# Kernel optimization log

Measured on AMD Instinct MI355X. Metric: run time of the kernel, lower is better.

The kernel has to match this reference:

```python
import jax, jax.numpy as jnp
import numpy as np

N_STATE = 256   # complex state size n (real state is 2n)
N_IN = 128
BATCH = 16
T_STEPS = 2048
H_STEP = 0.01
EPS = 1e-3
LAM_RE_MIN, LAM_RE_MAX, MAX_PHASE = -5.0, -0.5, 6.283


def setup_inputs() -> dict:
    rng = np.random.default_rng(0)
    n, nu = N_STATE, N_IN
    # trainable params (as in torch __init__)
    u1 = rng.random(n)
    u2 = rng.random(n) * 2.0 - 1.0
    alpha = np.log(-(u1 * (LAM_RE_MAX - LAM_RE_MIN) + LAM_RE_MIN)).astype(np.float32)
    theta = (MAX_PHASE * u2).astype(np.float32)
    B_re = (rng.standard_normal((n, nu)) / np.sqrt(2.0 * nu)).astype(np.float32)
    B_im = (rng.standard_normal((n, nu)) / np.sqrt(2.0 * nu)).astype(np.float32)
    # fixed basis-change buffers: rho (normalized), T_inv, P = rho @ T_inv, Pinv
    H1 = rng.standard_normal((n, n))
    H2 = rng.standard_normal((n, n))
    rho = np.block([[H1, -H2], [H2, H1]])
    rho = rho / np.linalg.norm(rho)
    I = np.eye(n)
    T_inv = (1.0 / np.sqrt(2.0)) * np.block([[I, I], [-1j * I, 1j * I]])
    P = rho.astype(np.complex128) @ T_inv
    Pinv = np.linalg.inv(P)
    key = jax.random.key(0)
    k1, k2 = jax.random.split(key)
    return {
        "xi_init": jax.random.normal(k1, (BATCH, 1, 2 * n), dtype=jnp.float32),
        "u_log": jax.random.normal(k2, (BATCH, T_STEPS, nu), dtype=jnp.float32),
        "alpha": jnp.asarray(alpha),
        "theta": jnp.asarray(theta),
        "B_re": jnp.asarray(B_re),
        "B_im": jnp.asarray(B_im),
        "P_re": jnp.asarray(P.real, dtype=jnp.float32),
        "P_im": jnp.asarray(P.imag, dtype=jnp.float32),
        "Pinv_re": jnp.asarray(Pinv.real, dtype=jnp.float32),
        "Pinv_im": jnp.asarray(Pinv.imag, dtype=jnp.float32),
        "T": T_STEPS,
    }


def reference(xi_init, u_log, alpha, theta, B_re, B_im, P_re, P_im, Pinv_re, Pinv_im, T):
    n = alpha.shape[0]
    lam = (-jnp.exp(alpha) - EPS) + 1j * theta          # (n,) complex64
    Bc = B_re + 1j * B_im                               # (n, nu)
    P = P_re + 1j * P_im                                # (2n, 2n)
    Pinv = Pinv_re + 1j * Pinv_im                       # (2n, 2n)
    xi0 = xi_init[:, 0, :]                              # (B, 2n) real

    def step(xi, u_t):
        # xi: (B, 2n) real state; u_t: (B, nu)
        x_tilde = xi.astype(jnp.complex64) @ Pinv.T     # (B, 2n) complex
        x_bar = x_tilde[:, :n]                          # (B, n)
        x_bar_dot = lam * x_bar + u_t.astype(jnp.complex64) @ Bc.T
        x_tilde_dot = jnp.concatenate([x_bar_dot, jnp.conj(x_bar_dot)], axis=-1)
        x_dot = (x_tilde_dot @ P.T).real                # (B, 2n)
        xi_new = xi + H_STEP * x_dot
        return xi_new, xi_new

    u_seq = jnp.swapaxes(u_log, 0, 1)                   # (T, B, nu)
    _, xs = jax.lax.scan(step, xi0, u_seq)              # (T, B, 2n)
    # torch _sim logs xi_init, then skips xi after t=0, logs xi after t=1..T-1
    x_log = jnp.concatenate([xi0[None], xs[1:]], axis=0)  # (T, B, 2n)
    return jnp.swapaxes(x_log, 0, 1)                    # (B, T, 2n)
```

## Files before the change

kernel.cpp:

```cpp
#include <hip/hip_runtime.h>
#include <hip/hip_bf16.h>
#include <cstddef>
#include <cstdint>

#define N_ST 256
#define TWO_N 512
#define NU 128
#define BATCH 16
#define TSTEPS 2048
#define MTOT (BATCH * TSTEPS)
#define H_STEP 0.01f
#define EPS_V 0.001f
#define NCHUNK 32
#define CHUNKL 64

typedef __attribute__((ext_vector_type(4))) float f32x4;
typedef __attribute__((ext_vector_type(4))) short s16x4;
typedef __attribute__((ext_vector_type(8))) short s16x8;

#define OFF_FPK    0
#define OFF_ZPK    8388608
#define OFF_UPK    16777216
#define OFF_WT     18874368
#define OFF_WF     19005440
#define OFF_D      19038208
#define OFF_XBAR0  19039232
#define OFF_E      19047424

static __device__ __forceinline__ float bf2f(short s) {
    return __uint_as_float(((unsigned)(unsigned short)s) << 16);
}

__global__ __launch_bounds__(256) void prep_all(
    const float* __restrict__ P_re, const float* __restrict__ P_im,
    const float* __restrict__ B_re, const float* __restrict__ B_im,
    const float* __restrict__ alpha, const float* __restrict__ theta,
    short* __restrict__ Wtpk, short* __restrict__ Wfpk,
    float* __restrict__ dbuf)
{
    int blk = blockIdx.x, tid = threadIdx.x;
    if (blk < 1024) {
        int idx = blk * 256 + tid;
        int j = idx >> 9, c = idx & 511;
        float v;
        if (c < N_ST) v = P_re[j * TWO_N + c] + P_re[j * TWO_N + c + N_ST];
        else          v = P_im[j * TWO_N + c] - P_im[j * TWO_N + c - N_ST];
        __hip_bfloat16 b = __float2bfloat16(v);
        Wtpk[((size_t)(j >> 4) * TWO_N + c) * 16 + (j & 15)] = *(short*)&b;
    } else if (blk < 1280) {
        int idx = (blk - 1024) * 256 + tid;
        int k = idx >> 9, c = idx & 511;
        float v = (c < N_ST) ? B_re[c * NU + k] : B_im[(c - N_ST) * NU + k];
        __hip_bfloat16 b = __float2bfloat16(H_STEP * v);
        Wfpk[((size_t)(c >> 4) * NU + k) * 16 + (c & 15)] = *(short*)&b;
    } else {
        int i = tid;
        float dr = 1.0f + H_STEP * (-expf(alpha[i]) - EPS_V);
        float di = H_STEP * theta[i];
        float pr = 1.0f, pi = 0.0f;
        for (int k = 0; k < CHUNKL; ++k) { float nr = pr * dr - pi * di; pi = pr * di + pi * dr; pr = nr; }
        dbuf[i] = dr; dbuf[N_ST + i] = di; dbuf[2 * N_ST + i] = pr; dbuf[3 * N_ST + i] = pi;
    }
}

__global__ __launch_bounds__(256) void xbar0_kernel(
    const float* __restrict__ Pinv_re, const float* __restrict__ Pinv_im,
    const float* __restrict__ xi0, float* __restrict__ xbar0)
{
    __shared__ float xs[BATCH * TWO_N];
    int tid = threadIdx.x;
#pragma unroll
    for (int q = 0; q < 8; ++q)
        *reinterpret_cast<float4*>(&xs[(q * 256 + tid) * 4]) =
            *reinterpret_cast<const float4*>(&xi0[(q * 256 + tid) * 4]);
    __syncthreads();

    int wv = tid >> 6, l = tid & 63;
    int i = blockIdx.x * 4 + wv;
    float rp[BATCH] = {}, ip[BATCH] = {};
#pragma unroll
    for (int q = 0; q < 8; ++q) {
        int j = q * 64 + l;
        float pr = Pinv_re[(size_t)i * TWO_N + j];
        float pi = Pinv_im[(size_t)i * TWO_N + j];
#pragma unroll
        for (int b = 0; b < BATCH; ++b) {
            float x = xs[b * TWO_N + j];
            rp[b] = fmaf(pr, x, rp[b]);
            ip[b] = fmaf(pi, x, ip[b]);
        }
    }
#pragma unroll
    for (int m = 1; m < 64; m <<= 1) {
#pragma unroll
        for (int b = 0; b < BATCH; ++b) {
            rp[b] += __shfl_xor(rp[b], m, 64);
            ip[b] += __shfl_xor(ip[b], m, 64);
        }
    }
    if (l == 0) {
#pragma unroll
        for (int b = 0; b < BATCH; ++b) {
            xbar0[b * TWO_N + i] = rp[b];
            xbar0[b * TWO_N + N_ST + i] = ip[b];
        }
    }
}

__global__ __launch_bounds__(256) void upack(const float* __restrict__ u, short* __restrict__ upk) {
    __shared__ short st[64 * 132];
    int tid = threadIdx.x, bid = blockIdx.x;
    const float* up = u + (size_t)bid * 8192;
#pragma unroll
    for (int q = 0; q < 8; ++q) {
        int idx = q * 1024 + tid * 4;
        float4 v = *reinterpret_cast<const float4*>(up + idx);
        int m = idx >> 7, k = idx & 127;
        s16x4 pv;
        __hip_bfloat16 b0 = __float2bfloat16(v.x); pv[0] = *(short*)&b0;
        __hip_bfloat16 b1 = __float2bfloat16(v.y); pv[1] = *(short*)&b1;
        __hip_bfloat16 b2 = __float2bfloat16(v.z); pv[2] = *(short*)&b2;
        __hip_bfloat16 b3 = __float2bfloat16(v.w); pv[3] = *(short*)&b3;
        *reinterpret_cast<__shared__ s16x4*>(&st[m * 132 + k]) = pv;
    }
    __syncthreads();
    short* op = upk + (size_t)bid * 8192;
#pragma unroll
    for (int q2 = 0; q2 < 4; ++q2) {
        int o = q2 * 2048 + tid * 8;
        int ml = o & 15, k = (o >> 4) & 127, sl = o >> 11;
        s16x8 w;
#pragma unroll
        for (int r = 0; r < 8; ++r) w[r] = st[(sl * 16 + ml + r) * 132 + k];
        *reinterpret_cast<s16x8*>(op + o) = w;
    }
}

template <int K, bool PACKOUT>
__global__ __launch_bounds__(512, 2) void gemm_mfma(const short* __restrict__ Apk,
                                                    const short* __restrict__ Bpk,
                                                    float* __restrict__ Cf,
                                                    short* __restrict__ Cp,
                                                    const float* __restrict__ xi0) {
    __shared__ __align__(1024) short lds[32768];
    const int tid = threadIdx.x;
    const int wid = tid >> 6, lane = tid & 63;
    const int l = blockIdx.x;
    const int mb = ((l >> 4) << 3) | (l & 7);
    const int nb = (l >> 3) & 1;
    const int m0 = mb * 256, n0 = nb * 256;
    const int wm = wid >> 2, wn = wid & 3;
    f32x4 acc[8][4] = {};
    const size_t slabStride = (size_t)K * 16;
    const unsigned ldsBase = (unsigned)(uintptr_t)(__attribute__((address_space(3))) short*)&lds[0];
    constexpr int NT = K / 32;

#define STAGE(buf, kk)                                                                              \
    do {                                                                                            \
        const short* gA0 = Apk + ((size_t)(m0 >> 4) + wid)     * slabStride + (size_t)(kk) * 16 + lane * 8; \
        const short* gA1 = Apk + ((size_t)(m0 >> 4) + wid + 8) * slabStride + (size_t)(kk) * 16 + lane * 8; \
        const short* gB0 = Bpk + ((size_t)(n0 >> 4) + wid)     * slabStride + (size_t)(kk) * 16 + lane * 8; \
        const short* gB1 = Bpk + ((size_t)(n0 >> 4) + wid + 8) * slabStride + (size_t)(kk) * 16 + lane * 8; \
        __builtin_amdgcn_global_load_lds((const __attribute__((address_space(1))) void*)gA0,        \
            (__attribute__((address_space(3))) void*)&lds[(buf) * 8192 + wid * 512], 16, 0, 0);     \
        __builtin_amdgcn_global_load_lds((const __attribute__((address_space(1))) void*)gA1,        \
            (__attribute__((address_space(3))) void*)&lds[(buf) * 8192 + (wid + 8) * 512], 16, 0, 0); \
        __builtin_amdgcn_global_load_lds((const __attribute__((address_space(1))) void*)gB0,        \
            (__attribute__((address_space(3))) void*)&lds[16384 + (buf) * 8192 + wid * 512], 16, 0, 0); \
        __builtin_amdgcn_global_load_lds((const __attribute__((address_space(1))) void*)gB1,        \
            (__attribute__((address_space(3))) void*)&lds[16384 + (buf) * 8192 + (wid + 8) * 512], 16, 0, 0); \
    } while (0)

    STAGE(0, 0);

#pragma unroll
    for (int t = 0; t < NT; ++t) {
        const int cur = t & 1;
        if (t + 1 < NT) STAGE(cur ^ 1, (t + 1) * 32);

        if (t + 1 < NT) asm volatile("s_waitcnt vmcnt(4)" ::: "memory");
        else            asm volatile("s_waitcnt vmcnt(0)" ::: "memory");
        __builtin_amdgcn_sched_barrier(0);
        __builtin_amdgcn_s_barrier();
        __builtin_amdgcn_sched_barrier(0);

        s16x4 al[8], ah[8], bl[4], bh[4];
        const unsigned aB = ldsBase + (unsigned)cur * 16384u;
        const unsigned bB = ldsBase + 32768u + (unsigned)cur * 16384u;
#pragma unroll
        for (int i = 0; i < 8; ++i) {
            unsigned ad = aB + ((unsigned)(wm * 8 + i) << 10) + ((unsigned)lane << 3);
            asm volatile("ds_read_b64_tr_b16 %0, %1 offset:0"   : "=v"(al[i]) : "v"(ad));
            asm volatile("ds_read_b64_tr_b16 %0, %1 offset:512" : "=v"(ah[i]) : "v"(ad));
        }
#pragma unroll
        for (int j = 0; j < 4; ++j) {
            unsigned bd = bB + ((unsigned)(wn * 4 + j) << 10) + ((unsigned)lane << 3);
            asm volatile("ds_read_b64_tr_b16 %0, %1 offset:0"   : "=v"(bl[j]) : "v"(bd));
            asm volatile("ds_read_b64_tr_b16 %0, %1 offset:512" : "=v"(bh[j]) : "v"(bd));
        }
        asm volatile("s_waitcnt lgkmcnt(0)" ::: "memory");
        __builtin_amdgcn_sched_barrier(0);
        __builtin_amdgcn_s_barrier();
        __builtin_amdgcn_sched_barrier(0);

        __builtin_amdgcn_s_setprio(1);
#pragma unroll
        for (int i = 0; i < 8; ++i) {
            s16x8 av = __builtin_shufflevector(al[i], ah[i], 0, 1, 2, 3, 4, 5, 6, 7);
#pragma unroll
            for (int j = 0; j < 4; ++j) {
                s16x8 bv = __builtin_shufflevector(bl[j], bh[j], 0, 1, 2, 3, 4, 5, 6, 7);
                acc[i][j] = __builtin_amdgcn_mfma_f32_16x16x32_bf16(av, bv, acc[i][j], 0, 0, 0);
            }
        }
        __builtin_amdgcn_s_setprio(0);
    }
#undef STAGE

    const int cn = lane & 15;
    const int g4 = (lane >> 4) * 4;
    if (!PACKOUT) {
#pragma unroll
        for (int i = 0; i < 8; ++i) {
            int mrow = m0 + wm * 128 + i * 16 + g4;
#pragma unroll
            for (int j = 0; j < 4; ++j) {
                int ncol = n0 + wn * 64 + j * 16 + cn;
                float* cp = Cf + (size_t)mrow * TWO_N + ncol;
#pragma unroll
                for (int r = 0; r < 4; ++r) {
                    float v = acc[i][j][r];
                    if (((mrow + r) & (TSTEPS - 1)) == 0)
                        v = xi0[((mrow + r) >> 11) * TWO_N + ncol];
                    cp[(size_t)r * TWO_N] = v;
                }
            }
        }
    } else {
#pragma unroll
        for (int i = 0; i < 8; ++i) {
            size_t slab = (size_t)((m0 >> 4) + wm * 8 + i);
#pragma unroll
            for (int j = 0; j < 4; ++j) {
                int n = n0 + wn * 64 + j * 16 + cn;
                s16x4 pv;
#pragma unroll
                for (int r = 0; r < 4; ++r) {
                    __hip_bfloat16 bb = __float2bfloat16(acc[i][j][r]);
                    pv[r] = *reinterpret_cast<short*>(&bb);
                }
                *reinterpret_cast<s16x4*>(Cp + slab * 8192 + (size_t)n * 16 + g4) = pv;
            }
        }
    }
}

__global__ __launch_bounds__(256) void scan_passA(const short* __restrict__ Fpk,
                                                  const float* __restrict__ dbuf,
                                                  float* __restrict__ e) {
    int b = blockIdx.x, c = blockIdx.y, i = threadIdx.x;
    float dr = dbuf[i], di = dbuf[N_ST + i];
    float re = 0.f, im = 0.f;
    int slab0 = (b * TSTEPS + c * CHUNKL) >> 4;
#pragma unroll
    for (int g = 0; g < 4; ++g) {
        const short* base = Fpk + (size_t)(slab0 + g) * 8192 + i * 16;
        s16x8 r0 = *reinterpret_cast<const s16x8*>(base);
        s16x8 r1 = *reinterpret_cast<const s16x8*>(base + 8);
        s16x8 i0 = *reinterpret_cast<const s16x8*>(base + 4096);
        s16x8 i1 = *reinterpret_cast<const s16x8*>(base + 4096 + 8);
#pragma unroll
        for (int j = 0; j < 16; ++j) {
            float fr = bf2f(j < 8 ? r0[j & 7] : r1[j & 7]);
            float fi = bf2f(j < 8 ? i0[j & 7] : i1[j & 7]);
            float nre = fmaf(dr, re, fmaf(-di, im, fr));
            float nim = fmaf(dr, im, fmaf(di, re, fi));
            re = nre; im = nim;
        }
    }
    size_t o = ((size_t)(b * NCHUNK + c)) * TWO_N;
    e[o + i] = re;
    e[o + N_ST + i] = im;
}

__global__ __launch_bounds__(256) void scan_passC(const short* __restrict__ Fpk,
                                                  const float* __restrict__ dbuf,
                                                  const float* __restrict__ e,
                                                  const float* __restrict__ xbar0,
                                                  short* __restrict__ Zpk) {
    int b = blockIdx.x, c = blockIdx.y, i = threadIdx.x;
    float dr = dbuf[i], di = dbuf[N_ST + i];
    float dLr = dbuf[2 * N_ST + i], dLi = dbuf[3 * N_ST + i];
    float re = xbar0[b * TWO_N + i], im = xbar0[b * TWO_N + N_ST + i];
    for (int cc = 0; cc < c; ++cc) {
        size_t o = ((size_t)(b * NCHUNK + cc)) * TWO_N;
        float er = e[o + i], ei = e[o + N_ST + i];
        float nre = fmaf(dLr, re, fmaf(-dLi, im, er));
        float nim = fmaf(dLr, im, fmaf(dLi, re, ei));
        re = nre; im = nim;
    }
    int slab0 = (b * TSTEPS + c * CHUNKL) >> 4;
#pragma unroll
    for (int g = 0; g < 4; ++g) {
        const short* base = Fpk + (size_t)(slab0 + g) * 8192 + i * 16;
        s16x8 r0 = *reinterpret_cast<const s16x8*>(base);
        s16x8 r1 = *reinterpret_cast<const s16x8*>(base + 8);
        s16x8 i0 = *reinterpret_cast<const s16x8*>(base + 4096);
        s16x8 i1 = *reinterpret_cast<const s16x8*>(base + 4096 + 8);
        s16x8 zr0, zr1, zi0, zi1;
#pragma unroll
        for (int j = 0; j < 16; ++j) {
            float fr = bf2f(j < 8 ? r0[j & 7] : r1[j & 7]);
            float fi = bf2f(j < 8 ? i0[j & 7] : i1[j & 7]);
            float nre = fmaf(dr, re, fmaf(-di, im, fr));
            float nim = fmaf(dr, im, fmaf(di, re, fi));
            re = nre; im = nim;
            __hip_bfloat16 br = __float2bfloat16(re), bi = __float2bfloat16(im);
            if (j < 8) { zr0[j & 7] = *(short*)&br; zi0[j & 7] = *(short*)&bi; }
            else       { zr1[j & 7] = *(short*)&br; zi1[j & 7] = *(short*)&bi; }
        }
        short* zb = Zpk + (size_t)(slab0 + g) * 8192 + i * 16;
        *reinterpret_cast<s16x8*>(zb)            = zr0;
        *reinterpret_cast<s16x8*>(zb + 8)        = zr1;
        *reinterpret_cast<s16x8*>(zb + 4096)     = zi0;
        *reinterpret_cast<s16x8*>(zb + 4096 + 8) = zi1;
    }
}

extern "C" void kernel_launch(void* const* d_in, const int* in_sizes, int n_in,
                              void* d_out, int out_size, void* d_ws, size_t ws_size,
                              hipStream_t stream) {
    const float* xi_init = (const float*)d_in[0];
    const float* u_log   = (const float*)d_in[1];
    const float* alpha   = (const float*)d_in[2];
    const float* theta   = (const float*)d_in[3];
    const float* B_re    = (const float*)d_in[4];
    const float* B_im    = (const float*)d_in[5];
    const float* P_re    = (const float*)d_in[6];
    const float* P_im    = (const float*)d_in[7];
    const float* Pinv_re = (const float*)d_in[8];
    const float* Pinv_im = (const float*)d_in[9];
    float* out = (float*)d_out;
    float* ws  = (float*)d_ws;

    short* Fpk  = (short*)(ws + OFF_FPK);
    short* Zpk  = (short*)(ws + OFF_ZPK);
    short* upk  = (short*)(ws + OFF_UPK);
    short* Wtpk = (short*)(ws + OFF_WT);
    short* Wfpk = (short*)(ws + OFF_WF);
    float* dbuf  = ws + OFF_D;
    float* xbar0 = ws + OFF_XBAR0;
    float* e     = ws + OFF_E;

    prep_all<<<1281, 256, 0, stream>>>(P_re, P_im, B_re, B_im, alpha, theta,
                                       Wtpk, Wfpk, dbuf);
    xbar0_kernel<<<64, 256, 0, stream>>>(Pinv_re, Pinv_im, xi_init, xbar0);
    upack<<<MTOT / 64, 256, 0, stream>>>(u_log, upk);

    gemm_mfma<NU, true><<<256, 512, 0, stream>>>(
        upk, Wfpk, nullptr, Fpk, nullptr);

    scan_passA<<<dim3(BATCH, NCHUNK), 256, 0, stream>>>(Fpk, dbuf, e);
    scan_passC<<<dim3(BATCH, NCHUNK), 256, 0, stream>>>(Fpk, dbuf, e, xbar0, Zpk);

    gemm_mfma<TWO_N, false><<<256, 512, 0, stream>>>(
        Zpk, Wtpk, out, nullptr, xi_init);
}
```

Baseline: 80.08 us.

## Interleave GEMM global-to-LDS prefetch with per-phase LDS reads and MFMA

Restructures the MFMA GEMM main loop into four phases per K-tile. Each phase issues one of the four global_load_lds prefetches for the next tile, reads two A fragments, and runs eight MFMAs, where before all loads, reads and MFMAs ran as separate blocks. The goal is to spread memory issue across the compute, shorten the time each LDS-read burst stalls, and cut register pressure from holding all A fragments at once. In exchange it adds a workgroup barrier per phase and replaces the full unroll with unroll 2.

```diff
diff --git a/kernel.cpp b/kernel.cpp
--- a/kernel.cpp
+++ b/kernel.cpp
@@ -155,68 +155,94 @@
     const unsigned ldsBase = (unsigned)(uintptr_t)(__attribute__((address_space(3))) short*)&lds[0];
     constexpr int NT = K / 32;
 
-#define STAGE(buf, kk)                                                                              \
+#define STAGE1(buf, kk, p)                                                                          \
     do {                                                                                            \
-        const short* gA0 = Apk + ((size_t)(m0 >> 4) + wid)     * slabStride + (size_t)(kk) * 16 + lane * 8; \
-        const short* gA1 = Apk + ((size_t)(m0 >> 4) + wid + 8) * slabStride + (size_t)(kk) * 16 + lane * 8; \
-        const short* gB0 = Bpk + ((size_t)(n0 >> 4) + wid)     * slabStride + (size_t)(kk) * 16 + lane * 8; \
-        const short* gB1 = Bpk + ((size_t)(n0 >> 4) + wid + 8) * slabStride + (size_t)(kk) * 16 + lane * 8; \
-        __builtin_amdgcn_global_load_lds((const __attribute__((address_space(1))) void*)gA0,        \
-            (__attribute__((address_space(3))) void*)&lds[(buf) * 8192 + wid * 512], 16, 0, 0);     \
-        __builtin_amdgcn_global_load_lds((const __attribute__((address_space(1))) void*)gA1,        \
-            (__attribute__((address_space(3))) void*)&lds[(buf) * 8192 + (wid + 8) * 512], 16, 0, 0); \
-        __builtin_amdgcn_global_load_lds((const __attribute__((address_space(1))) void*)gB0,        \
-            (__attribute__((address_space(3))) void*)&lds[16384 + (buf) * 8192 + wid * 512], 16, 0, 0); \
-        __builtin_amdgcn_global_load_lds((const __attribute__((address_space(1))) void*)gB1,        \
-            (__attribute__((address_space(3))) void*)&lds[16384 + (buf) * 8192 + (wid + 8) * 512], 16, 0, 0); \
+        const bool isA_ = (p) < 2;                                                                  \
+        const int r_ = ((p) & 1) ? wid + 8 : wid;                                                   \
+        const short* src_ = (isA_ ? Apk + ((size_t)(m0 >> 4) + r_) * slabStride                     \
+                                  : Bpk + ((size_t)(n0 >> 4) + r_) * slabStride)                    \
+                            + (size_t)(kk) * 16 + lane * 8;                                         \
+        __builtin_amdgcn_global_load_lds((const __attribute__((address_space(1))) void*)src_,       \
+            (__attribute__((address_space(3))) void*)&lds[(isA_ ? 0 : 16384) + (buf) * 8192 + r_ * 512], \
+            16, 0, 0);                                                                              \
     } while (0)
 
-    STAGE(0, 0);
-
-#pragma unroll
+    STAGE1(0, 0, 0); STAGE1(0, 0, 1); STAGE1(0, 0, 2); STAGE1(0, 0, 3);
+
+#pragma unroll 2
     for (int t = 0; t < NT; ++t) {
         const int cur = t & 1;
-        if (t + 1 < NT) STAGE(cur ^ 1, (t + 1) * 32);
-
-        if (t + 1 < NT) asm volatile("s_waitcnt vmcnt(4)" ::: "memory");
-        else            asm volatile("s_waitcnt vmcnt(0)" ::: "memory");
+        const unsigned aB = ldsBase + (unsigned)cur * 16384u;
+        const unsigned bB = ldsBase + 32768u + (unsigned)cur * 16384u;
+        s16x8 bv[4];
+
+        if (t + 1 < NT) {
+            STAGE1(cur ^ 1, (t + 1) * 32, 0);
+            asm volatile("s_waitcnt vmcnt(1)" ::: "memory");
+        } else {
+            asm volatile("s_waitcnt vmcnt(0)" ::: "memory");
+        }
         __builtin_amdgcn_sched_barrier(0);
         __builtin_amdgcn_s_barrier();
         __builtin_amdgcn_sched_barrier(0);
-
-        s16x4 al[8], ah[8], bl[4], bh[4];
-        const unsigned aB = ldsBase + (unsigned)cur * 16384u;
-        const unsigned bB = ldsBase + 32768u + (unsigned)cur * 16384u;
-#pragma unroll
-        for (int i = 0; i < 8; ++i) {
-            unsigned ad = aB + ((unsigned)(wm * 8 + i) << 10) + ((unsigned)lane << 3);
-            asm volatile("ds_read_b64_tr_b16 %0, %1 offset:0"   : "=v"(al[i]) : "v"(ad));
-            asm volatile("ds_read_b64_tr_b16 %0, %1 offset:512" : "=v"(ah[i]) : "v"(ad));
-        }
-#pragma unroll
-        for (int j = 0; j < 4; ++j) {
-            unsigned bd = bB + ((unsigned)(wn * 4 + j) << 10) + ((unsigned)lane << 3);
-            asm volatile("ds_read_b64_tr_b16 %0, %1 offset:0"   : "=v"(bl[j]) : "v"(bd));
-            asm volatile("ds_read_b64_tr_b16 %0, %1 offset:512" : "=v"(bh[j]) : "v"(bd));
-        }
-        asm volatile("s_waitcnt lgkmcnt(0)" ::: "memory");
-        __builtin_amdgcn_sched_barrier(0);
+        {
+            s16x4 bl[4], bh[4], a0l, a0h, a1l, a1h;
+#pragma unroll
+            for (int j = 0; j < 4; ++j) {
+                unsigned bd = bB + ((unsigned)(wn * 4 + j) << 10) + ((unsigned)lane << 3);
+                asm volatile("ds_read_b64_tr_b16 %0, %1 offset:0"   : "=v"(bl[j]) : "v"(bd));
+                asm volatile("ds_read_b64_tr_b16 %0, %1 offset:512" : "=v"(bh[j]) : "v"(bd));
+            }
+            unsigned ad0 = aB + ((unsigned)(wm * 8 + 0) << 10) + ((unsigned)lane << 3);
+            unsigned ad1 = aB + ((unsigned)(wm * 8 + 1) << 10) + ((unsigned)lane << 3);
+            asm volatile("ds_read_b64_tr_b16 %0, %1 offset:0"   : "=v"(a0l) : "v"(ad0));
+            asm volatile("ds_read_b64_tr_b16 %0, %1 offset:512" : "=v"(a0h) : "v"(ad0));
+            asm volatile("ds_read_b64_tr_b16 %0, %1 offset:0"   : "=v"(a1l) : "v"(ad1));
+            asm volatile("ds_read_b64_tr_b16 %0, %1 offset:512" : "=v"(a1h) : "v"(ad1));
+            asm volatile("s_waitcnt lgkmcnt(0)" ::: "memory");
+            __builtin_amdgcn_sched_barrier(0);
+#pragma unroll
+            for (int j = 0; j < 4; ++j)
+                bv[j] = __builtin_shufflevector(bl[j], bh[j], 0, 1, 2, 3, 4, 5, 6, 7);
+            s16x8 a0 = __builtin_shufflevector(a0l, a0h, 0, 1, 2, 3, 4, 5, 6, 7);
+            s16x8 a1 = __builtin_shufflevector(a1l, a1h, 0, 1, 2, 3, 4, 5, 6, 7);
+            __builtin_amdgcn_s_setprio(1);
+#pragma unroll
+            for (int j = 0; j < 4; ++j) {
+                acc[0][j] = __builtin_amdgcn_mfma_f32_16x16x32_bf16(a0, bv[j], acc[0][j], 0, 0, 0);
+                acc[1][j] = __builtin_amdgcn_mfma_f32_16x16x32_bf16(a1, bv[j], acc[1][j], 0, 0, 0);
+            }
+            __builtin_amdgcn_s_setprio(0);
+        }
         __builtin_amdgcn_s_barrier();
         __builtin_amdgcn_sched_barrier(0);
 
-        __builtin_amdgcn_s_setprio(1);
-#pragma unroll
-        for (int i = 0; i < 8; ++i) {
-            s16x8 av = __builtin_shufflevector(al[i], ah[i], 0, 1, 2, 3, 4, 5, 6, 7);
-#pragma unroll
-            for (int j = 0; j < 4; ++j) {
-                s16x8 bv = __builtin_shufflevector(bl[j], bh[j], 0, 1, 2, 3, 4, 5, 6, 7);
-                acc[i][j] = __builtin_amdgcn_mfma_f32_16x16x32_bf16(av, bv, acc[i][j], 0, 0, 0);
-            }
-        }
-        __builtin_amdgcn_s_setprio(0);
-    }
-#undef STAGE
+#pragma unroll
+        for (int p = 1; p < 4; ++p) {
+            if (t + 1 < NT) STAGE1(cur ^ 1, (t + 1) * 32, p);
+            s16x4 a0l, a0h, a1l, a1h;
+            unsigned ad0 = aB + ((unsigned)(wm * 8 + 2 * p) << 10) + ((unsigned)lane << 3);
+            unsigned ad1 = aB + ((unsigned)(wm * 8 + 2 * p + 1) << 10) + ((unsigned)lane << 3);
+            asm volatile("ds_read_b64_tr_b16 %0, %1 offset:0"   : "=v"(a0l) : "v"(ad0));
+            asm volatile("ds_read_b64_tr_b16 %0, %1 offset:512" : "=v"(a0h) : "v"(ad0));
+            asm volatile("ds_read_b64_tr_b16 %0, %1 offset:0"   : "=v"(a1l) : "v"(ad1));
+            asm volatile("ds_read_b64_tr_b16 %0, %1 offset:512" : "=v"(a1h) : "v"(ad1));
+            asm volatile("s_waitcnt lgkmcnt(0)" ::: "memory");
+            __builtin_amdgcn_sched_barrier(0);
+            s16x8 a0 = __builtin_shufflevector(a0l, a0h, 0, 1, 2, 3, 4, 5, 6, 7);
+            s16x8 a1 = __builtin_shufflevector(a1l, a1h, 0, 1, 2, 3, 4, 5, 6, 7);
+            __builtin_amdgcn_s_setprio(1);
+#pragma unroll
+            for (int j = 0; j < 4; ++j) {
+                acc[2 * p][j]     = __builtin_amdgcn_mfma_f32_16x16x32_bf16(a0, bv[j], acc[2 * p][j], 0, 0, 0);
+                acc[2 * p + 1][j] = __builtin_amdgcn_mfma_f32_16x16x32_bf16(a1, bv[j], acc[2 * p + 1][j], 0, 0, 0);
+            }
+            __builtin_amdgcn_s_setprio(0);
+            __builtin_amdgcn_s_barrier();
+            __builtin_amdgcn_sched_barrier(0);
+        }
+    }
+#undef STAGE1
 
     const int cn = lane & 15;
     const int g4 = (lane >> 4) * 4;
```

Result: slower. 81.97 us (+2.4%).

## Fuse prep kernels into one launch and triple-buffer GEMM LDS staging

Applied to the files above, without the earlier changes.

Merges the prep, xbar0 and u-packing kernels into a single launch, with block-index ranges dispatching to each task. This removes two kernel launches and their serialization gaps. The MFMA GEMM moves from double to triple buffering of its LDS tiles, prefetching two K-steps ahead with adjusted vmcnt waits to hide global load latency. LDS per block grows to 96KB, which may reduce blocks resident per CU.

```diff
diff --git a/kernel.cpp b/kernel.cpp
--- a/kernel.cpp
+++ b/kernel.cpp
@@ -31,13 +31,17 @@
     return __uint_as_float(((unsigned)(unsigned short)s) << 16);
 }
 
-__global__ __launch_bounds__(256) void prep_all(
+__global__ __launch_bounds__(256) void prep_mega(
     const float* __restrict__ P_re, const float* __restrict__ P_im,
     const float* __restrict__ B_re, const float* __restrict__ B_im,
     const float* __restrict__ alpha, const float* __restrict__ theta,
+    const float* __restrict__ Pinv_re, const float* __restrict__ Pinv_im,
+    const float* __restrict__ xi0, const float* __restrict__ u,
     short* __restrict__ Wtpk, short* __restrict__ Wfpk,
-    float* __restrict__ dbuf)
+    float* __restrict__ dbuf, float* __restrict__ xbar0,
+    short* __restrict__ upk)
 {
+    __shared__ float xs[BATCH * TWO_N];
     int blk = blockIdx.x, tid = threadIdx.x;
     if (blk < 1024) {
         int idx = blk * 256 + tid;
@@ -53,86 +57,76 @@
         float v = (c < N_ST) ? B_re[c * NU + k] : B_im[(c - N_ST) * NU + k];
         __hip_bfloat16 b = __float2bfloat16(H_STEP * v);
         Wfpk[((size_t)(c >> 4) * NU + k) * 16 + (c & 15)] = *(short*)&b;
-    } else {
+    } else if (blk == 1280) {
         int i = tid;
         float dr = 1.0f + H_STEP * (-expf(alpha[i]) - EPS_V);
         float di = H_STEP * theta[i];
         float pr = 1.0f, pi = 0.0f;
         for (int k = 0; k < CHUNKL; ++k) { float nr = pr * dr - pi * di; pi = pr * di + pi * dr; pr = nr; }
         dbuf[i] = dr; dbuf[N_ST + i] = di; dbuf[2 * N_ST + i] = pr; dbuf[3 * N_ST + i] = pi;
-    }
-}
-
-__global__ __launch_bounds__(256) void xbar0_kernel(
-    const float* __restrict__ Pinv_re, const float* __restrict__ Pinv_im,
-    const float* __restrict__ xi0, float* __restrict__ xbar0)
-{
-    __shared__ float xs[BATCH * TWO_N];
-    int tid = threadIdx.x;
-#pragma unroll
-    for (int q = 0; q < 8; ++q)
-        *reinterpret_cast<float4*>(&xs[(q * 256 + tid) * 4]) =
-            *reinterpret_cast<const float4*>(&xi0[(q * 256 + tid) * 4]);
-    __syncthreads();
-
-    int wv = tid >> 6, l = tid & 63;
-    int i = blockIdx.x * 4 + wv;
-    float rp[BATCH] = {}, ip[BATCH] = {};
-#pragma unroll
-    for (int q = 0; q < 8; ++q) {
-        int j = q * 64 + l;
-        float pr = Pinv_re[(size_t)i * TWO_N + j];
-        float pi = Pinv_im[(size_t)i * TWO_N + j];
-#pragma unroll
-        for (int b = 0; b < BATCH; ++b) {
-            float x = xs[b * TWO_N + j];
-            rp[b] = fmaf(pr, x, rp[b]);
-            ip[b] = fmaf(pi, x, ip[b]);
-        }
-    }
-#pragma unroll
-    for (int m = 1; m < 64; m <<= 1) {
-#pragma unroll
-        for (int b = 0; b < BATCH; ++b) {
-            rp[b] += __shfl_xor(rp[b], m, 64);
-            ip[b] += __shfl_xor(ip[b], m, 64);
-        }
-    }
-    if (l == 0) {
-#pragma unroll
-        for (int b = 0; b < BATCH; ++b) {
-            xbar0[b * TWO_N + i] = rp[b];
-            xbar0[b * TWO_N + N_ST + i] = ip[b];
-        }
-    }
-}
-
-__global__ __launch_bounds__(256) void upack(const float* __restrict__ u, short* __restrict__ upk) {
-    __shared__ short st[64 * 132];
-    int tid = threadIdx.x, bid = blockIdx.x;
-    const float* up = u + (size_t)bid * 8192;
-#pragma unroll
-    for (int q = 0; q < 8; ++q) {
-        int idx = q * 1024 + tid * 4;
-        float4 v = *reinterpret_cast<const float4*>(up + idx);
-        int m = idx >> 7, k = idx & 127;
-        s16x4 pv;
-        __hip_bfloat16 b0 = __float2bfloat16(v.x); pv[0] = *(short*)&b0;
-        __hip_bfloat16 b1 = __float2bfloat16(v.y); pv[1] = *(short*)&b1;
-        __hip_bfloat16 b2 = __float2bfloat16(v.z); pv[2] = *(short*)&b2;
-        __hip_bfloat16 b3 = __float2bfloat16(v.w); pv[3] = *(short*)&b3;
-        *reinterpret_cast<__shared__ s16x4*>(&st[m * 132 + k]) = pv;
-    }
-    __syncthreads();
-    short* op = upk + (size_t)bid * 8192;
-#pragma unroll
-    for (int q2 = 0; q2 < 4; ++q2) {
-        int o = q2 * 2048 + tid * 8;
-        int ml = o & 15, k = (o >> 4) & 127, sl = o >> 11;
-        s16x8 w;
-#pragma unroll
-        for (int r = 0; r < 8; ++r) w[r] = st[(sl * 16 + ml + r) * 132 + k];
-        *reinterpret_cast<s16x8*>(op + o) = w;
+    } else if (blk < 1345) {
+#pragma unroll
+        for (int q = 0; q < 8; ++q)
+            *reinterpret_cast<float4*>(&xs[(q * 256 + tid) * 4]) =
+                *reinterpret_cast<const float4*>(&xi0[(q * 256 + tid) * 4]);
+        __syncthreads();
+        int wv = tid >> 6, l = tid & 63;
+        int i = (blk - 1281) * 4 + wv;
+        float rp[BATCH] = {}, ip[BATCH] = {};
+#pragma unroll
+        for (int q = 0; q < 8; ++q) {
+            int j = q * 64 + l;
+            float pr = Pinv_re[(size_t)i * TWO_N + j];
+            float pi = Pinv_im[(size_t)i * TWO_N + j];
+#pragma unroll
+            for (int b = 0; b < BATCH; ++b) {
+                float x = xs[b * TWO_N + j];
+                rp[b] = fmaf(pr, x, rp[b]);
+                ip[b] = fmaf(pi, x, ip[b]);
+            }
+        }
+#pragma unroll
+        for (int m = 1; m < 64; m <<= 1) {
+#pragma unroll
+            for (int b = 0; b < BATCH; ++b) {
+                rp[b] += __shfl_xor(rp[b], m, 64);
+                ip[b] += __shfl_xor(ip[b], m, 64);
+            }
+        }
+        if (l == 0) {
+#pragma unroll
+            for (int b = 0; b < BATCH; ++b) {
+                xbar0[b * TWO_N + i] = rp[b];
+                xbar0[b * TWO_N + N_ST + i] = ip[b];
+            }
+        }
+    } else {
+        short* st = (short*)xs;
+        int bid = blk - 1345;
+        const float* up = u + (size_t)bid * 8192;
+#pragma unroll
+        for (int q = 0; q < 8; ++q) {
+            int idx = q * 1024 + tid * 4;
+            float4 v = *reinterpret_cast<const float4*>(up + idx);
+            int m = idx >> 7, k = idx & 127;
+            s16x4 pv;
+            __hip_bfloat16 b0 = __float2bfloat16(v.x); pv[0] = *(short*)&b0;
+            __hip_bfloat16 b1 = __float2bfloat16(v.y); pv[1] = *(short*)&b1;
+            __hip_bfloat16 b2 = __float2bfloat16(v.z); pv[2] = *(short*)&b2;
+            __hip_bfloat16 b3 = __float2bfloat16(v.w); pv[3] = *(short*)&b3;
+            *reinterpret_cast<__shared__ s16x4*>(&st[m * 132 + k]) = pv;
+        }
+        __syncthreads();
+        short* op = upk + (size_t)bid * 8192;
+#pragma unroll
+        for (int q2 = 0; q2 < 4; ++q2) {
+            int o = q2 * 2048 + tid * 8;
+            int ml = o & 15, k = (o >> 4) & 127, sl = o >> 11;
+            s16x8 w;
+#pragma unroll
+            for (int r = 0; r < 8; ++r) w[r] = st[(sl * 16 + ml + r) * 132 + k];
+            *reinterpret_cast<s16x8*>(op + o) = w;
+        }
     }
 }
 
@@ -142,7 +136,7 @@
                                                     float* __restrict__ Cf,
                                                     short* __restrict__ Cp,
                                                     const float* __restrict__ xi0) {
-    __shared__ __align__(1024) short lds[32768];
+    __shared__ __align__(1024) short lds[49152];
     const int tid = threadIdx.x;
     const int wid = tid >> 6, lane = tid & 63;
     const int l = blockIdx.x;
@@ -166,27 +160,29 @@
         __builtin_amdgcn_global_load_lds((const __attribute__((address_space(1))) void*)gA1,        \
             (__attribute__((address_space(3))) void*)&lds[(buf) * 8192 + (wid + 8) * 512], 16, 0, 0); \
         __builtin_amdgcn_global_load_lds((const __attribute__((address_space(1))) void*)gB0,        \
-            (__attribute__((address_space(3))) void*)&lds[16384 + (buf) * 8192 + wid * 512], 16, 0, 0); \
+            (__attribute__((address_space(3))) void*)&lds[24576 + (buf) * 8192 + wid * 512], 16, 0, 0); \
         __builtin_amdgcn_global_load_lds((const __attribute__((address_space(1))) void*)gB1,        \
-            (__attribute__((address_space(3))) void*)&lds[16384 + (buf) * 8192 + (wid + 8) * 512], 16, 0, 0); \
+            (__attribute__((address_space(3))) void*)&lds[24576 + (buf) * 8192 + (wid + 8) * 512], 16, 0, 0); \
     } while (0)
 
     STAGE(0, 0);
+    STAGE(1, 32);
 
 #pragma unroll
     for (int t = 0; t < NT; ++t) {
-        const int cur = t & 1;
-        if (t + 1 < NT) STAGE(cur ^ 1, (t + 1) * 32);
-
-        if (t + 1 < NT) asm volatile("s_waitcnt vmcnt(4)" ::: "memory");
-        else            asm volatile("s_waitcnt vmcnt(0)" ::: "memory");
+        const int cur = t % 3;
+        if (t + 2 < NT) STAGE((t + 2) % 3, (t + 2) * 32);
+
+        if (t + 2 < NT)      asm volatile("s_waitcnt vmcnt(8)" ::: "memory");
+        else if (t + 1 < NT) asm volatile("s_waitcnt vmcnt(4)" ::: "memory");
+        else                 asm volatile("s_waitcnt vmcnt(0)" ::: "memory");
         __builtin_amdgcn_sched_barrier(0);
         __builtin_amdgcn_s_barrier();
         __builtin_amdgcn_sched_barrier(0);
 
         s16x4 al[8], ah[8], bl[4], bh[4];
         const unsigned aB = ldsBase + (unsigned)cur * 16384u;
-        const unsigned bB = ldsBase + 32768u + (unsigned)cur * 16384u;
+        const unsigned bB = ldsBase + 49152u + (unsigned)cur * 16384u;
 #pragma unroll
         for (int i = 0; i < 8; ++i) {
             unsigned ad = aB + ((unsigned)(wm * 8 + i) << 10) + ((unsigned)lane << 3);
@@ -353,10 +349,9 @@
     float* xbar0 = ws + OFF_XBAR0;
     float* e     = ws + OFF_E;
 
-    prep_all<<<1281, 256, 0, stream>>>(P_re, P_im, B_re, B_im, alpha, theta,
-                                       Wtpk, Wfpk, dbuf);
-    xbar0_kernel<<<64, 256, 0, stream>>>(Pinv_re, Pinv_im, xi_init, xbar0);
-    upack<<<MTOT / 64, 256, 0, stream>>>(u_log, upk);
+    prep_mega<<<1857, 256, 0, stream>>>(P_re, P_im, B_re, B_im, alpha, theta,
+                                        Pinv_re, Pinv_im, xi_init, u_log,
+                                        Wtpk, Wfpk, dbuf, xbar0, upk);
 
     gemm_mfma<NU, true><<<256, 512, 0, stream>>>(
         upk, Wfpk, nullptr, Fpk, nullptr);
```

Measured after the change: 73.58 us. 1.09x faster.
